# Kernel optimization log

Hardware: AMD Instinct MI355X
Metric: run time of the kernel (lower is better)

## Reference

```python
import math
import jax, jax.numpy as jnp
import numpy as np

N_NODES = 50000
N_EDGES = 800000
FEAT = 64          # m * p == p * n == 64
P = 8              # product_size
M = FEAT // P      # 8


def setup_inputs() -> dict:
    key = jax.random.key(0)
    k1, k2, k3, k4 = jax.random.split(key, 4)
    src_feat = jax.random.normal(k1, (N_NODES, FEAT), dtype=jnp.float32)
    dst_feat = jax.random.normal(k2, (N_NODES, FEAT), dtype=jnp.float32)
    edge_src = jax.random.randint(k3, (N_EDGES,), 0, N_NODES, dtype=jnp.int32)
    edge_dst = jax.random.randint(k4, (N_EDGES,), 0, N_NODES, dtype=jnp.int32)
    return {"src_feat": src_feat, "dst_feat": dst_feat,
            "edge_src": edge_src, "edge_dst": edge_dst}


def reference(src_feat, dst_feat, edge_src, edge_dst):
    # src.view(..., -1, P) ; dst.view(..., P, -1)
    src = src_feat.reshape(N_NODES, M, P)          # [N, m, p]
    dst = dst_feat.reshape(N_NODES, P, M)          # [N, p, n]
    # per-edge SDDMM-style batched matmul: gather endpoints, matmul
    e_src = src[edge_src]                          # [E, m, p]
    e_dst = dst[edge_dst]                          # [E, p, n]
    ft_e = jnp.einsum('eij,ejk->eik', e_src, e_dst)  # [E, m, n]
    # sum-aggregate edge features onto destination nodes
    agg = jax.ops.segment_sum(ft_e, edge_dst, num_segments=N_NODES)  # [N, m, n]
    result = agg / math.sqrt(P)
    # squeeze: flatten last two dims
    return result.reshape(N_NODES, M * M)
```

## Files before the change

### kernel.cpp

```cpp
#include <hip/hip_runtime.h>
#include <hip/hip_bf16.h>

#define N_NODES 50000
#define N_EDGES 800000
#define FEAT 64
#define RANGE 32
#define NBINS 1563
#define K1B 250
#define EPB (N_EDGES / K1B)
#define SUB 16
#define RSTRIDE 4096
#define CAPP 48
#define BSTRIDE 52
#define DUMMY N_NODES

static __device__ __forceinline__ unsigned short f2bu(float f) {
    __hip_bfloat16 h = __float2bfloat16(f);
    return __builtin_bit_cast(unsigned short, h);
}

__global__ __launch_bounds__(256) void conv_kernel(
    const float* __restrict__ src_feat,
    unsigned short* __restrict__ src16)
{
    int base = (blockIdx.x * 256 + threadIdx.x) * 8;
    if (base >= (N_NODES + 1) * FEAT) return;
    uint4 o;
    if (base < N_NODES * FEAT) {
        float4 a = *(const float4*)(src_feat + base);
        float4 b = *(const float4*)(src_feat + base + 4);
        o.x = (unsigned)f2bu(a.x) | ((unsigned)f2bu(a.y) << 16);
        o.y = (unsigned)f2bu(a.z) | ((unsigned)f2bu(a.w) << 16);
        o.z = (unsigned)f2bu(b.x) | ((unsigned)f2bu(b.y) << 16);
        o.w = (unsigned)f2bu(b.z) | ((unsigned)f2bu(b.w) << 16);
    } else {
        o = make_uint4(0, 0, 0, 0);
    }
    *(uint4*)(src16 + base) = o;
}

__global__ __launch_bounds__(256) void bin_kernel(
    const int* __restrict__ edge_src,
    const int* __restrict__ edge_dst,
    int* __restrict__ counts,
    int* __restrict__ ent)
{
    __shared__ int h[NBINS];
    int tid = threadIdx.x;
    int b = blockIdx.x;
    int e0 = b * EPB;
    int e1 = e0 + EPB;

    for (int r = tid; r < NBINS; r += 256) h[r] = 0;
    __syncthreads();

    for (int e = e0 + tid * 4; e < e1; e += 1024) {
        int4 s4 = *(const int4*)(edge_src + e);
        int4 d4 = *(const int4*)(edge_dst + e);
        int r0 = d4.x >> 5, r1 = d4.y >> 5, r2 = d4.z >> 5, r3 = d4.w >> 5;
        int p0 = atomicAdd(&h[r0], 1);
        int p1 = atomicAdd(&h[r1], 1);
        int p2 = atomicAdd(&h[r2], 1);
        int p3 = atomicAdd(&h[r3], 1);
        if (p0 < SUB) ent[r0 * RSTRIDE + b * SUB + p0] = ((d4.x & 31) << 16) | s4.x;
        if (p1 < SUB) ent[r1 * RSTRIDE + b * SUB + p1] = ((d4.y & 31) << 16) | s4.y;
        if (p2 < SUB) ent[r2 * RSTRIDE + b * SUB + p2] = ((d4.z & 31) << 16) | s4.z;
        if (p3 < SUB) ent[r3 * RSTRIDE + b * SUB + p3] = ((d4.w & 31) << 16) | s4.w;
    }
    __syncthreads();

    for (int r = tid; r < NBINS; r += 256) {
        int c = h[r];
        counts[b * NBINS + r] = (c > SUB) ? SUB : c;
    }
}

__global__ __launch_bounds__(512, 8) void sort_gather_mm_kernel(
    const unsigned short* __restrict__ src16,
    const float* __restrict__ dst_feat,
    const int* __restrict__ counts,
    const int* __restrict__ ent,
    float* __restrict__ out)
{
    __shared__ int bucket_w[RANGE * BSTRIDE];
    __shared__ int cnt_s[256];
    __shared__ int c[RANGE];

    int r = blockIdx.x;
    int tid = threadIdx.x;
    int wave = tid >> 6;
    int lane = tid & 63;

    const int* er = ent + (size_t)r * RSTRIDE;
    int ew[8];
    #pragma unroll
    for (int k = 0; k < 8; ++k)
        ew[k] = er[tid + k * 512];

    if (tid < 256) cnt_s[tid] = (tid < K1B) ? counts[tid * NBINS + r] : 0;
    if (tid < RANGE) c[tid] = 0;

    float Bv[4];
    #pragma unroll
    for (int m = 0; m < 4; ++m) {
        int n = r * RANGE + wave * 4 + m;
        Bv[m] = (n < N_NODES) ? dst_feat[n * FEAT + lane] : 0.f;
    }
    __syncthreads();

    #pragma unroll
    for (int k = 0; k < 8; ++k) {
        int g = tid + k * 512;
        int bb = g >> 4;
        int s  = g & 15;
        if (s < cnt_s[bb]) {
            int p = ew[k];
            int dl = p >> 16;
            int pos = atomicAdd(&c[dl], 1);
            if (pos < CAPP) bucket_w[dl * BSTRIDE + pos] = p & 0xFFFF;
        }
    }
    __syncthreads();

    if (tid < RANGE) {
        int cc = c[tid]; if (cc > CAPP) cc = CAPP;
        while (cc & 3) bucket_w[tid * BSTRIDE + cc++] = DUMMY;
        c[tid] = cc >> 2;
    }
    __syncthreads();

    int sub = lane >> 4;
    int fc  = lane & 15;
    int rows4[4], qmax = 0;
    #pragma unroll
    for (int m = 0; m < 4; ++m) {
        rows4[m] = c[wave * 4 + m];
        qmax = (rows4[m] > qmax) ? rows4[m] : qmax;
    }

    float acc[4][4] = {{0.f,0.f,0.f,0.f},{0.f,0.f,0.f,0.f},
                       {0.f,0.f,0.f,0.f},{0.f,0.f,0.f,0.f}};
    for (int q = 0; q < qmax; ++q) {
        uint2 L[4];
        #pragma unroll
        for (int m = 0; m < 4; ++m) {
            int nl = wave * 4 + m;
            int raw = bucket_w[nl * BSTRIDE + q * 4 + sub];
            int id = (q < rows4[m]) ? raw : DUMMY;
            L[m] = *(const uint2*)(src16 + (size_t)id * FEAT + fc * 4);
        }
        #pragma unroll
        for (int m = 0; m < 4; ++m) {
            acc[m][0] += __uint_as_float(L[m].x << 16);
            acc[m][1] += __uint_as_float(L[m].x & 0xFFFF0000u);
            acc[m][2] += __uint_as_float(L[m].y << 16);
            acc[m][3] += __uint_as_float(L[m].y & 0xFFFF0000u);
        }
    }

    #pragma unroll
    for (int m = 0; m < 4; ++m) {
        #pragma unroll
        for (int u = 0; u < 4; ++u) {
            acc[m][u] += __shfl_xor(acc[m][u], 16, 64);
            acc[m][u] += __shfl_xor(acc[m][u], 32, 64);
        }
    }

    int i = lane >> 3;
    int j = lane & 7;
    #pragma unroll
    for (int m = 0; m < 4; ++m) {
        int n = r * RANGE + wave * 4 + m;
        if (n >= N_NODES) break;
        float res = 0.0f;
        #pragma unroll
        for (int p = 0; p < 8; ++p) {
            float s_ip = __shfl(acc[m][p & 3], 2 * i + (p >> 2), 64);
            float b_pj = __shfl(Bv[m], p * 8 + j, 64);
            res += s_ip * b_pj;
        }
        out[n * FEAT + lane] = res * 0.35355339059327373f;
    }
}

extern "C" void kernel_launch(void* const* d_in, const int* in_sizes, int n_in,
                              void* d_out, int out_size, void* d_ws, size_t ws_size,
                              hipStream_t stream) {
    const float* src_feat = (const float*)d_in[0];
    const float* dst_feat = (const float*)d_in[1];
    const int* edge_src = (const int*)d_in[2];
    const int* edge_dst = (const int*)d_in[3];
    float* out = (float*)d_out;

    char* w = (char*)d_ws;
    int* counts = (int*)w;                        w += 1563008;
    int* ent = (int*)w;                           w += (size_t)NBINS * RSTRIDE * 4;
    unsigned short* src16 = (unsigned short*)w;

    int blocksConv = ((N_NODES + 1) * FEAT / 8 + 255) / 256;
    conv_kernel<<<blocksConv, 256, 0, stream>>>(src_feat, src16);

    bin_kernel<<<K1B, 256, 0, stream>>>(edge_src, edge_dst, counts, ent);

    sort_gather_mm_kernel<<<NBINS, 512, 0, stream>>>(
        src16, dst_feat, counts, ent, out);
}
```

Before: 116.6 us.

## Fuse conversion and binning kernels, software-pipeline gather loads in aggregation

Merges the bf16 conversion kernel and the edge binning kernel into one launch with 1024-thread blocks, where the first blocks convert and the rest bin, so one launch and its gap disappear. The gather/accumulate loop in the main kernel is double-buffered so the next iteration's index reads and global loads are issued before the current accumulation, aiming to hide gather latency. The min-blocks hint in launch bounds drops from 8 to 6 to leave registers for the extra buffers, at the cost of possibly lower occupancy.

```diff
diff --git a/kernel.cpp b/kernel.cpp
--- a/kernel.cpp
+++ b/kernel.cpp
@@ -13,33 +13,16 @@
 #define CAPP 48
 #define BSTRIDE 52
 #define DUMMY N_NODES
+#define CONVB 391
 
 static __device__ __forceinline__ unsigned short f2bu(float f) {
     __hip_bfloat16 h = __float2bfloat16(f);
     return __builtin_bit_cast(unsigned short, h);
 }
 
-__global__ __launch_bounds__(256) void conv_kernel(
+__global__ __launch_bounds__(1024) void conv_bin_kernel(
     const float* __restrict__ src_feat,
-    unsigned short* __restrict__ src16)
-{
-    int base = (blockIdx.x * 256 + threadIdx.x) * 8;
-    if (base >= (N_NODES + 1) * FEAT) return;
-    uint4 o;
-    if (base < N_NODES * FEAT) {
-        float4 a = *(const float4*)(src_feat + base);
-        float4 b = *(const float4*)(src_feat + base + 4);
-        o.x = (unsigned)f2bu(a.x) | ((unsigned)f2bu(a.y) << 16);
-        o.y = (unsigned)f2bu(a.z) | ((unsigned)f2bu(a.w) << 16);
-        o.z = (unsigned)f2bu(b.x) | ((unsigned)f2bu(b.y) << 16);
-        o.w = (unsigned)f2bu(b.z) | ((unsigned)f2bu(b.w) << 16);
-    } else {
-        o = make_uint4(0, 0, 0, 0);
-    }
-    *(uint4*)(src16 + base) = o;
-}
-
-__global__ __launch_bounds__(256) void bin_kernel(
+    unsigned short* __restrict__ src16,
     const int* __restrict__ edge_src,
     const int* __restrict__ edge_dst,
     int* __restrict__ counts,
@@ -47,14 +30,31 @@
 {
     __shared__ int h[NBINS];
     int tid = threadIdx.x;
-    int b = blockIdx.x;
-    int e0 = b * EPB;
-    int e1 = e0 + EPB;
-
-    for (int r = tid; r < NBINS; r += 256) h[r] = 0;
-    __syncthreads();
-
-    for (int e = e0 + tid * 4; e < e1; e += 1024) {
+
+    if (blockIdx.x < CONVB) {
+        int base = (blockIdx.x * 1024 + tid) * 8;
+        if (base >= (N_NODES + 1) * FEAT) return;
+        uint4 o;
+        if (base < N_NODES * FEAT) {
+            float4 a = *(const float4*)(src_feat + base);
+            float4 b = *(const float4*)(src_feat + base + 4);
+            o.x = (unsigned)f2bu(a.x) | ((unsigned)f2bu(a.y) << 16);
+            o.y = (unsigned)f2bu(a.z) | ((unsigned)f2bu(a.w) << 16);
+            o.z = (unsigned)f2bu(b.x) | ((unsigned)f2bu(b.y) << 16);
+            o.w = (unsigned)f2bu(b.z) | ((unsigned)f2bu(b.w) << 16);
+        } else {
+            o = make_uint4(0, 0, 0, 0);
+        }
+        *(uint4*)(src16 + base) = o;
+        return;
+    }
+
+    int b = blockIdx.x - CONVB;
+    for (int r = tid; r < NBINS; r += 1024) h[r] = 0;
+    __syncthreads();
+
+    if (tid < EPB / 4) {
+        int e = b * EPB + tid * 4;
         int4 s4 = *(const int4*)(edge_src + e);
         int4 d4 = *(const int4*)(edge_dst + e);
         int r0 = d4.x >> 5, r1 = d4.y >> 5, r2 = d4.z >> 5, r3 = d4.w >> 5;
@@ -69,13 +69,32 @@
     }
     __syncthreads();
 
-    for (int r = tid; r < NBINS; r += 256) {
+    for (int r = tid; r < NBINS; r += 1024) {
         int c = h[r];
         counts[b * NBINS + r] = (c > SUB) ? SUB : c;
     }
 }
 
-__global__ __launch_bounds__(512, 8) void sort_gather_mm_kernel(
+#define RDIDX(ID, Q)                                                          \
+    _Pragma("unroll")                                                         \
+    for (int m_ = 0; m_ < 4; ++m_) {                                          \
+        int raw_ = bucket_w[(wave * 4 + m_) * BSTRIDE + (Q) * 4 + sub];       \
+        ID[m_] = ((Q) < rows4[m_]) ? raw_ : DUMMY;                            \
+    }
+#define GLOAD(L, ID)                                                          \
+    _Pragma("unroll")                                                         \
+    for (int m_ = 0; m_ < 4; ++m_)                                            \
+        L[m_] = *(const uint2*)(src16 + (size_t)ID[m_] * FEAT + fc * 4);
+#define ACCUM(L)                                                              \
+    _Pragma("unroll")                                                         \
+    for (int m_ = 0; m_ < 4; ++m_) {                                          \
+        acc[m_][0] += __uint_as_float(L[m_].x << 16);                         \
+        acc[m_][1] += __uint_as_float(L[m_].x & 0xFFFF0000u);                 \
+        acc[m_][2] += __uint_as_float(L[m_].y << 16);                         \
+        acc[m_][3] += __uint_as_float(L[m_].y & 0xFFFF0000u);                 \
+    }
+
+__global__ __launch_bounds__(512, 6) void sort_gather_mm_kernel(
     const unsigned short* __restrict__ src16,
     const float* __restrict__ dst_feat,
     const int* __restrict__ counts,
@@ -140,21 +159,21 @@
 
     float acc[4][4] = {{0.f,0.f,0.f,0.f},{0.f,0.f,0.f,0.f},
                        {0.f,0.f,0.f,0.f},{0.f,0.f,0.f,0.f}};
-    for (int q = 0; q < qmax; ++q) {
-        uint2 L[4];
-        #pragma unroll
-        for (int m = 0; m < 4; ++m) {
-            int nl = wave * 4 + m;
-            int raw = bucket_w[nl * BSTRIDE + q * 4 + sub];
-            int id = (q < rows4[m]) ? raw : DUMMY;
-            L[m] = *(const uint2*)(src16 + (size_t)id * FEAT + fc * 4);
-        }
-        #pragma unroll
-        for (int m = 0; m < 4; ++m) {
-            acc[m][0] += __uint_as_float(L[m].x << 16);
-            acc[m][1] += __uint_as_float(L[m].x & 0xFFFF0000u);
-            acc[m][2] += __uint_as_float(L[m].y << 16);
-            acc[m][3] += __uint_as_float(L[m].y & 0xFFFF0000u);
+    {
+        int idA[4], idB[4];
+        uint2 LA[4], LB[4];
+        if (qmax > 0) { RDIDX(idA, 0); GLOAD(LA, idA); }
+        int q = 0;
+        while (q < qmax) {
+            int qn = q + 1;
+            if (qn < qmax) { RDIDX(idB, qn); GLOAD(LB, idB); }
+            ACCUM(LA);
+            q = qn;
+            if (q >= qmax) break;
+            qn = q + 1;
+            if (qn < qmax) { RDIDX(idA, qn); GLOAD(LA, idA); }
+            ACCUM(LB);
+            q = qn;
         }
     }
 
@@ -198,10 +217,8 @@
     int* ent = (int*)w;                           w += (size_t)NBINS * RSTRIDE * 4;
     unsigned short* src16 = (unsigned short*)w;
 
-    int blocksConv = ((N_NODES + 1) * FEAT / 8 + 255) / 256;
-    conv_kernel<<<blocksConv, 256, 0, stream>>>(src_feat, src16);
-
-    bin_kernel<<<K1B, 256, 0, stream>>>(edge_src, edge_dst, counts, ent);
+    conv_bin_kernel<<<CONVB + K1B, 1024, 0, stream>>>(
+        src_feat, src16, edge_src, edge_dst, counts, ent);
 
     sort_gather_mm_kernel<<<NBINS, 512, 0, stream>>>(
         src16, dst_feat, counts, ent, out);
```

Measured after the change: 115.7 us. About the same (-0.8%).
